# Kernel optimization log

Measured on AMD Instinct MI355X. Metric: run time of the kernel, lower is better.

## Reference

```python
import jax, jax.numpy as jnp
import numpy as np

B, S, DIM, H = 2, 2048, 2048, 16
HD = DIM // H  # head_dim = 128
EPS = 1e-6


def setup_inputs() -> dict:
    key = jax.random.key(0)
    ks = jax.random.split(key, 13)
    d = {
        'hidden_states': jax.random.normal(ks[0], (B, S, DIM), jnp.float32),
        'freqs_cos': jax.random.normal(ks[1], (1, S, 1, HD), jnp.float32),
        'freqs_sin': jax.random.normal(ks[2], (1, S, 1, HD), jnp.float32),
        'Wq': jax.random.normal(ks[3], (DIM, DIM), jnp.float32) * 0.02,
        'bq': jax.random.normal(ks[4], (DIM,), jnp.float32) * 0.02,
        'Wk': jax.random.normal(ks[5], (DIM, DIM), jnp.float32) * 0.02,
        'bk': jax.random.normal(ks[6], (DIM,), jnp.float32) * 0.02,
        'Wv': jax.random.normal(ks[7], (DIM, DIM), jnp.float32) * 0.02,
        'bv': jax.random.normal(ks[8], (DIM,), jnp.float32) * 0.02,
        'norm_q_w': jax.random.uniform(ks[9], (DIM,), jnp.float32, 0.5, 1.5),
        'norm_k_w': jax.random.uniform(ks[10], (DIM,), jnp.float32, 0.5, 1.5),
        'Wo': jax.random.normal(ks[11], (DIM, DIM), jnp.float32) * 0.02,
        'bo': jax.random.normal(ks[12], (DIM,), jnp.float32) * 0.02,
    }
    return d


def _rms_norm(x, w, eps=EPS):
    # local RMSNorm over the full inner_dim (no cross-rank reduce)
    xf = x.astype(jnp.float32)
    var = jnp.mean(xf * xf, axis=-1, keepdims=True)
    return (w * (xf * jax.lax.rsqrt(var + eps))).astype(x.dtype)


def _apply_rope(x, freqs_cos, freqs_sin):
    # x: [B,H,S,D]; freqs: [1,S,1,D] -> broadcast cos/sin at [1,1,S,D/2]
    dtype = x.dtype
    xf = x.astype(jnp.float32)
    x1 = xf[..., 0::2]
    x2 = xf[..., 1::2]
    cos = jnp.transpose(freqs_cos[..., 0::2], (0, 2, 1, 3)).astype(jnp.float32)
    sin = jnp.transpose(freqs_sin[..., 1::2], (0, 2, 1, 3)).astype(jnp.float32)
    even = x1 * cos - x2 * sin
    odd = x1 * sin + x2 * cos
    out = jnp.stack([even, odd], axis=-1).reshape(x.shape)
    return out.astype(dtype)


def reference(hidden_states, freqs_cos, freqs_sin, Wq, bq, Wk, bk, Wv, bv,
              norm_q_w, norm_k_w, Wo, bo):
    b, s, _ = hidden_states.shape
    q = hidden_states @ Wq.T + bq
    k = hidden_states @ Wk.T + bk
    v = hidden_states @ Wv.T + bv
    q = _rms_norm(q, norm_q_w)
    k = _rms_norm(k, norm_k_w)
    # [B,S,H*D] -> [B,H,S,D]
    q = q.reshape(b, s, H, HD).transpose(0, 2, 1, 3)
    k = k.reshape(b, s, H, HD).transpose(0, 2, 1, 3)
    v = v.reshape(b, s, H, HD).transpose(0, 2, 1, 3)
    q = _apply_rope(q, freqs_cos, freqs_sin)
    k = _apply_rope(k, freqs_cos, freqs_sin)
    # flash attention math (full, non-causal), scale = 1/sqrt(head_dim)
    scale = 1.0 / np.sqrt(HD).astype(np.float32)
    scores = jnp.einsum('bhqd,bhkd->bhqk', q, k) * scale
    attn = jax.nn.softmax(scores, axis=-1)
    out = jnp.einsum('bhqk,bhkd->bhqd', attn, v)
    out = out.transpose(0, 2, 1, 3).reshape(b, s, H * HD)
    return out @ Wo.T + bo
```

## Files before the change

### kernel.cpp

```cpp
#include <hip/hip_runtime.h>
#include <stdint.h>

#define DEVI __device__ __forceinline__

typedef __attribute__((ext_vector_type(8))) short bf16x8;
typedef __attribute__((ext_vector_type(4))) float f32x4;
typedef __attribute__((ext_vector_type(16))) float f32x16;
typedef __attribute__((ext_vector_type(4))) unsigned short u16x4;
typedef __attribute__((ext_vector_type(8))) unsigned short u16x8;

DEVI unsigned short f2bf(float f) {
    union { float f; unsigned u; } v; v.f = f;
    unsigned r = v.u + 0x7fffu + ((v.u >> 16) & 1u);
    return (unsigned short)(r >> 16);
}

DEVI unsigned cvtpk(float lo, float hi) {
    unsigned r;
    asm("v_cvt_pk_bf16_f32 %0, %1, %2" : "=v"(r) : "v"(lo), "v"(hi));
    return r;
}

DEVI void gload16(const void* g, void* lds) {
    __builtin_amdgcn_global_load_lds(
        (const __attribute__((address_space(1))) unsigned int*)(uintptr_t)g,
        (__attribute__((address_space(3))) unsigned int*)(unsigned int)(uintptr_t)lds,
        16, 0, 0);
}

__global__ __launch_bounds__(256) void cvt_all(
    const float* __restrict__ hs, const float* __restrict__ wq,
    const float* __restrict__ wk, const float* __restrict__ wv,
    const float* __restrict__ wo,
    unsigned short* __restrict__ o_hs, unsigned short* __restrict__ o_wq,
    unsigned short* __restrict__ o_wk, unsigned short* __restrict__ o_wv,
    unsigned short* __restrict__ o_wo) {
    const int bid = blockIdx.x;
    const float* src; unsigned short* dst; int base;
    if (bid < 2048)      { src = hs; dst = o_hs; base = bid; }
    else if (bid < 3072) { src = wq; dst = o_wq; base = bid - 2048; }
    else if (bid < 4096) { src = wk; dst = o_wk; base = bid - 3072; }
    else if (bid < 5120) { src = wv; dst = o_wv; base = bid - 4096; }
    else                 { src = wo; dst = o_wo; base = bid - 5120; }
    const int i0 = base * 1024 + threadIdx.x;
#pragma unroll
    for (int k = 0; k < 4; k++) {
        const int i = i0 + k * 256;
        float4 v = ((const float4*)src)[i];
        u16x4 pk;
        pk[0] = f2bf(v.x); pk[1] = f2bf(v.y); pk[2] = f2bf(v.z); pk[3] = f2bf(v.w);
        ((u16x4*)dst)[i] = pk;
    }
}

DEVI void gemm_pipe_core(const unsigned short* __restrict__ A,
                         const unsigned short* __restrict__ Wt,
                         int m0, int n0, char* lds,
                         f32x4 (&acc)[2][2][2][2]) {
    constexpr int K = 2048;
    const int t = threadIdx.x;
    const int w = t >> 6, l = t & 63, lr = l & 15, lk = l >> 4;
    const int wr = w >> 2, wc = w & 3;
    const int sx = lr & 7;
    const int srow = t >> 3, sseg = (t & 7) ^ (srow & 7);
    const unsigned short* aS = A + (size_t)(m0 + srow) * K + sseg * 8;
    const unsigned short* bS = Wt + (size_t)(n0 + srow) * K + sseg * 8;
    char* Bbase = lds + 32768;

#pragma unroll
    for (int qm = 0; qm < 2; qm++)
#pragma unroll
        for (int qn = 0; qn < 2; qn++)
#pragma unroll
            for (int fr = 0; fr < 2; fr++)
#pragma unroll
                for (int fc = 0; fc < 2; fc++)
                    acc[qm][qn][fr][fc] = (f32x4){0.f, 0.f, 0.f, 0.f};

    auto STAGE = [&](int tt, int u) {
        if (tt >= 32) return;
        const int k0 = tt * 64, bb = tt & 1;
        if (u < 4)
            gload16(bS + (size_t)u * 64 * K + k0, Bbase + bb * 32768 + u * 8192 + w * 1024);
        else
            gload16(aS + (size_t)(u - 4) * 64 * K + k0, lds + bb * 16384 + (u - 4) * 8192 + w * 1024);
    };

    STAGE(0, 0); STAGE(0, 1); STAGE(0, 2); STAGE(0, 3); STAGE(0, 4); STAGE(0, 5);
    STAGE(1, 0); STAGE(1, 1); STAGE(1, 2);
    asm volatile("s_waitcnt vmcnt(3)" ::: "memory");
    __builtin_amdgcn_s_barrier();

    for (int kt = 0; kt < 32; ++kt) {
        const int bb = kt & 1;
        const char* Ab = lds + bb * 16384;
        const char* Bb = Bbase + bb * 32768;
        bf16x8 a0[2][2], a1[2][2], b0[2][2], b1[2][2];
#pragma unroll
        for (int fr = 0; fr < 2; fr++)
#pragma unroll
            for (int ks = 0; ks < 2; ks++) {
                a0[fr][ks] = *(const bf16x8*)(Ab + (wr * 64 + fr * 16 + lr) * 128 +
                                              (((ks * 4 + lk) ^ sx) << 4));
                a1[fr][ks] = *(const bf16x8*)(Ab + (wr * 64 + 32 + fr * 16 + lr) * 128 +
                                              (((ks * 4 + lk) ^ sx) << 4));
            }
#pragma unroll
        for (int fc = 0; fc < 2; fc++)
#pragma unroll
            for (int ks = 0; ks < 2; ks++) {
                b0[fc][ks] = *(const bf16x8*)(Bb + (wc * 64 + fc * 16 + lr) * 128 +
                                              (((ks * 4 + lk) ^ sx) << 4));
                b1[fc][ks] = *(const bf16x8*)(Bb + (wc * 64 + 32 + fc * 16 + lr) * 128 +
                                              (((ks * 4 + lk) ^ sx) << 4));
            }
        STAGE(kt + 1, 3); STAGE(kt + 1, 4); STAGE(kt + 1, 5);
        __builtin_amdgcn_s_setprio(1);
#pragma unroll
        for (int ks = 0; ks < 2; ks++)
#pragma unroll
            for (int fr = 0; fr < 2; fr++)
#pragma unroll
                for (int fc = 0; fc < 2; fc++) {
                    acc[0][0][fr][fc] = __builtin_amdgcn_mfma_f32_16x16x32_bf16(
                        a0[fr][ks], b0[fc][ks], acc[0][0][fr][fc], 0, 0, 0);
                    acc[1][0][fr][fc] = __builtin_amdgcn_mfma_f32_16x16x32_bf16(
                        a1[fr][ks], b0[fc][ks], acc[1][0][fr][fc], 0, 0, 0);
                }
        __builtin_amdgcn_s_setprio(0);
        asm volatile("s_waitcnt lgkmcnt(0)" ::: "memory");
        __builtin_amdgcn_s_barrier();
        STAGE(kt + 2, 0); STAGE(kt + 2, 1); STAGE(kt + 2, 2);
        __builtin_amdgcn_s_setprio(1);
#pragma unroll
        for (int ks = 0; ks < 2; ks++)
#pragma unroll
            for (int fr = 0; fr < 2; fr++)
#pragma unroll
                for (int fc = 0; fc < 2; fc++) {
                    acc[0][1][fr][fc] = __builtin_amdgcn_mfma_f32_16x16x32_bf16(
                        a0[fr][ks], b1[fc][ks], acc[0][1][fr][fc], 0, 0, 0);
                    acc[1][1][fr][fc] = __builtin_amdgcn_mfma_f32_16x16x32_bf16(
                        a1[fr][ks], b1[fc][ks], acc[1][1][fr][fc], 0, 0, 0);
                }
        __builtin_amdgcn_s_setprio(0);
        if (kt < 30)       asm volatile("s_waitcnt vmcnt(3)" ::: "memory");
        else if (kt == 30) asm volatile("s_waitcnt vmcnt(0)" ::: "memory");
        __builtin_amdgcn_s_barrier();
    }
}

__global__ __launch_bounds__(512, 2) void gemm_qkv(
    const unsigned short* __restrict__ A,
    const unsigned short* __restrict__ Wq16, const unsigned short* __restrict__ Wk16,
    const unsigned short* __restrict__ Wv16,
    const float* __restrict__ bq, const float* __restrict__ bk, const float* __restrict__ bv,
    float* __restrict__ qf, float* __restrict__ kf, unsigned short* __restrict__ Vt) {
    __shared__ char Lds[98304];
    const int bid = blockIdx.x;
    const int nt = bid & 7, rem = bid >> 3;
    const int mt = rem / 3, z = rem % 3;
    const int m0 = mt * 128, n0 = nt * 256;
    const unsigned short* W = (z == 0) ? Wq16 : (z == 1) ? Wk16 : Wv16;
    const float* bias = (z == 0) ? bq : (z == 1) ? bk : bv;

    f32x4 acc[2][2][2][2];
    gemm_pipe_core(A, W, m0, n0, Lds, acc);

    const int t = threadIdx.x, w = t >> 6, l = t & 63, lr = l & 15, lk = l >> 4;
    const int wr = w >> 2, wc = w & 3;
#pragma unroll
    for (int qm = 0; qm < 2; qm++)
#pragma unroll
        for (int qn = 0; qn < 2; qn++)
#pragma unroll
            for (int fr = 0; fr < 2; fr++)
#pragma unroll
                for (int fc = 0; fc < 2; fc++) {
                    const int col = n0 + wc * 64 + qn * 32 + fc * 16 + lr;
                    const int rb = m0 + wr * 64 + qm * 32 + fr * 16 + lk * 4;
                    const float bb = bias[col];
                    if (z == 2) {
                        const int hh = col >> 7, d = col & 127;
                        const int b = rb >> 11, s = rb & 2047;
                        u16x4 pk;
#pragma unroll
                        for (int j = 0; j < 4; j++) pk[j] = f2bf(acc[qm][qn][fr][fc][j] + bb);
                        *(u16x4*)(Vt + ((size_t)((b * 16 + hh) * 128 + d)) * 2048 + s) = pk;
                    } else {
                        float* out = (z == 0) ? qf : kf;
#pragma unroll
                        for (int j = 0; j < 4; j++)
                            out[(size_t)(rb + j) * 2048 + col] = acc[qm][qn][fr][fc][j] + bb;
                    }
                }
}

__global__ __launch_bounds__(512, 2) void gemm_o(
    const unsigned short* __restrict__ A, const unsigned short* __restrict__ W16,
    const float* __restrict__ bo, float* __restrict__ out) {
    __shared__ char Lds[98304];
    const int bid = blockIdx.x;
    const int nt = bid & 7, mt = bid >> 3;
    const int m0 = mt * 128, n0 = nt * 256;

    f32x4 acc[2][2][2][2];
    gemm_pipe_core(A, W16, m0, n0, Lds, acc);

    const int t = threadIdx.x, w = t >> 6, l = t & 63, lr = l & 15, lk = l >> 4;
    const int wr = w >> 2, wc = w & 3;
#pragma unroll
    for (int qm = 0; qm < 2; qm++)
#pragma unroll
        for (int qn = 0; qn < 2; qn++)
#pragma unroll
            for (int fr = 0; fr < 2; fr++)
#pragma unroll
                for (int fc = 0; fc < 2; fc++) {
                    const int col = n0 + wc * 64 + qn * 32 + fc * 16 + lr;
                    const int rb = m0 + wr * 64 + qm * 32 + fr * 16 + lk * 4;
                    const float bb = bo[col];
#pragma unroll
                    for (int j = 0; j < 4; j++)
                        out[(size_t)(rb + j) * 2048 + col] = acc[qm][qn][fr][fc][j] + bb;
                }
}

__global__ __launch_bounds__(256) void norm_rope(
    const float* __restrict__ qf, const float* __restrict__ kf,
    const float* __restrict__ nqw, const float* __restrict__ nkw,
    const float* __restrict__ fc, const float* __restrict__ fs,
    unsigned short* __restrict__ Qr, unsigned short* __restrict__ Kr) {
    const int row = blockIdx.x;
    const int which = blockIdx.y;
    const float* in = which ? kf : qf;
    const float* wv = which ? nkw : nqw;
    unsigned short* out = which ? Kr : Qr;
    const float qs = which ? 1.0f : 0.12751744f;
    const int t = threadIdx.x;
    const float* x = in + (size_t)row * 2048 + t * 8;
    float4 v0 = ((const float4*)x)[0];
    float4 v1 = ((const float4*)x)[1];
    float xv[8] = {v0.x, v0.y, v0.z, v0.w, v1.x, v1.y, v1.z, v1.w};
    float ss = 0.f;
#pragma unroll
    for (int e = 0; e < 8; e++) ss += xv[e] * xv[e];
#pragma unroll
    for (int m = 1; m < 64; m <<= 1) ss += __shfl_xor(ss, m, 64);
    __shared__ float red[4];
    if ((t & 63) == 0) red[t >> 6] = ss;
    __syncthreads();
    const float tot = red[0] + red[1] + red[2] + red[3];
    const float r = rsqrtf(tot * (1.0f / 2048.0f) + 1e-6f);
    const int s = row & 2047, b = row >> 11;
    const int d0 = t * 8, hd0 = d0 & 127, h = d0 >> 7;
    float4 c0 = ((const float4*)(fc + s * 128 + hd0))[0];
    float4 c1 = ((const float4*)(fc + s * 128 + hd0))[1];
    float4 s0 = ((const float4*)(fs + s * 128 + hd0))[0];
    float4 s1 = ((const float4*)(fs + s * 128 + hd0))[1];
    float4 w0 = ((const float4*)(wv + d0))[0];
    float4 w1 = ((const float4*)(wv + d0))[1];
    float wn[8] = {w0.x, w0.y, w0.z, w0.w, w1.x, w1.y, w1.z, w1.w};
    float xn[8];
#pragma unroll
    for (int e = 0; e < 8; e++) xn[e] = xv[e] * wn[e] * r;
    float o[8];
    o[0] = xn[0] * c0.x - xn[1] * s0.y;  o[1] = xn[0] * s0.y + xn[1] * c0.x;
    o[2] = xn[2] * c0.z - xn[3] * s0.w;  o[3] = xn[2] * s0.w + xn[3] * c0.z;
    o[4] = xn[4] * c1.x - xn[5] * s1.y;  o[5] = xn[4] * s1.y + xn[5] * c1.x;
    o[6] = xn[6] * c1.z - xn[7] * s1.w;  o[7] = xn[6] * s1.w + xn[7] * c1.z;
    u16x8 pk;
#pragma unroll
    for (int e = 0; e < 8; e++) pk[e] = f2bf(o[e] * qs);
    *(u16x8*)(out + ((size_t)((b * 16 + h) * 2048 + s)) * 128 + hd0) = pk;
}

__global__ __launch_bounds__(256, 2) void attn(
    const unsigned short* __restrict__ Qr, const unsigned short* __restrict__ Kr,
    const unsigned short* __restrict__ Vt, unsigned short* __restrict__ Ao) {
    __shared__ unsigned short Kl[2][64 * 128];
    __shared__ unsigned short Vl[2][128 * 64];
    const int t = threadIdx.x, w = t >> 6, l = t & 63;
    const int ql = l & 31, h = l >> 5;
    const int bid = blockIdx.x;
    const int xcd = bid & 7, idx = bid >> 3;
    const int bh = xcd * 4 + (idx >> 4);
    const int q0 = (idx & 15) * 128 + w * 32;
    const int b = bh >> 4, head = bh & 15;

    const unsigned short* Qp = Qr + ((size_t)bh * 2048 + q0) * 128;
    bf16x8 qf[8];
#pragma unroll
    for (int c8 = 0; c8 < 8; c8++)
        qf[c8] = *(const bf16x8*)(Qp + ql * 128 + c8 * 16 + h * 8);

    f32x16 accO[4];
#pragma unroll
    for (int dt = 0; dt < 4; dt++)
#pragma unroll
        for (int r = 0; r < 16; r++) accO[dt][r] = 0.f;
    float mj = -1e30f, ljp = 0.f;

    const unsigned short* Kb = Kr + (size_t)bh * 2048 * 128;
    const unsigned short* Vb = Vt + (size_t)bh * 128 * 2048;
    const int krow = t >> 4, kseg = (t & 15) ^ (krow & 7);
    const int vrow = t >> 3, vseg = (t & 7) ^ (vrow & 7);

    auto STAGE = [&](int buf, int kv0) {
        char* kd = (char*)&Kl[buf][0] + w * 1024;
        char* vd = (char*)&Vl[buf][0] + w * 1024;
#pragma unroll
        for (int c = 0; c < 4; c++)
            gload16(Kb + (size_t)(kv0 + c * 16 + krow) * 128 + kseg * 8, kd + c * 4096);
#pragma unroll
        for (int c = 0; c < 4; c++)
            gload16(Vb + (size_t)(c * 32 + vrow) * 2048 + kv0 + vseg * 8, vd + c * 4096);
    };

    const int qx = ql & 7;
    STAGE(0, 0);
    __syncthreads();
    int cur = 0;
    for (int it = 0; it < 32; ++it) {
        if (it < 31) STAGE(cur ^ 1, (it + 1) * 64);
        f32x16 S0, S1;
#pragma unroll
        for (int r = 0; r < 16; r++) { S0[r] = 0.f; S1[r] = 0.f; }
        __builtin_amdgcn_s_setprio(1);
#pragma unroll
        for (int c8 = 0; c8 < 8; c8++) {
            const int sg = ((c8 * 2 + h) ^ qx) << 4;
            bf16x8 k0 = *(const bf16x8*)((const char*)&Kl[cur][0] + ql * 256 + sg);
            bf16x8 k1 = *(const bf16x8*)((const char*)&Kl[cur][0] + (32 + ql) * 256 + sg);
            S0 = __builtin_amdgcn_mfma_f32_32x32x16_bf16(k0, qf[c8], S0, 0, 0, 0);
            S1 = __builtin_amdgcn_mfma_f32_32x32x16_bf16(k1, qf[c8], S1, 0, 0, 0);
        }
        __builtin_amdgcn_s_setprio(0);
        float mloc = S0[0];
#pragma unroll
        for (int r = 1; r < 16; r++) mloc = fmaxf(mloc, S0[r]);
#pragma unroll
        for (int r = 0; r < 16; r++) mloc = fmaxf(mloc, S1[r]);
        const float mx = fmaxf(mloc, __shfl_xor(mloc, 32, 64));
        if (!__all(mx <= mj + 8.0f)) {
            const float mn = fmaxf(mj, mx);
            const float corr = exp2f(mj - mn);
            mj = mn;
            ljp *= corr;
#pragma unroll
            for (int dt = 0; dt < 4; dt++)
#pragma unroll
                for (int r = 0; r < 16; r++) accO[dt][r] *= corr;
        }
        unsigned W[16];
        float lsum = 0.f;
#pragma unroll
        for (int i = 0; i < 8; i++) {
            const float pa = exp2f(S0[2 * i] - mj);
            const float pb = exp2f(S0[2 * i + 1] - mj);
            W[i] = cvtpk(pa, pb);
            lsum += pa + pb;
        }
#pragma unroll
        for (int i = 0; i < 8; i++) {
            const float pa = exp2f(S1[2 * i] - mj);
            const float pb = exp2f(S1[2 * i + 1] - mj);
            W[8 + i] = cvtpk(pa, pb);
            lsum += pa + pb;
        }
        ljp += lsum;
#pragma unroll
        for (int c = 0; c < 2; c++) {
            unsigned X[8];
#pragma unroll
            for (int i = 0; i < 8; i++)
                X[i] = (unsigned)__shfl_xor((int)W[c * 8 + i], 32, 64);
            union U { unsigned u[4]; bf16x8 v; };
            U F, G;
            F.u[0] = h ? X[2] : W[c * 8 + 0];
            F.u[1] = h ? X[3] : W[c * 8 + 1];
            F.u[2] = h ? W[c * 8 + 2] : X[0];
            F.u[3] = h ? W[c * 8 + 3] : X[1];
            G.u[0] = h ? X[6] : W[c * 8 + 4];
            G.u[1] = h ? X[7] : W[c * 8 + 5];
            G.u[2] = h ? W[c * 8 + 6] : X[4];
            G.u[3] = h ? W[c * 8 + 7] : X[5];
            __builtin_amdgcn_s_setprio(1);
#pragma unroll
            for (int dt = 0; dt < 4; dt++) {
                const int sg = (((2 * c) * 2 + h) ^ qx) << 4;
                bf16x8 vf = *(const bf16x8*)((const char*)&Vl[cur][0] + (dt * 32 + ql) * 128 + sg);
                accO[dt] = __builtin_amdgcn_mfma_f32_32x32x16_bf16(vf, F.v, accO[dt], 0, 0, 0);
            }
#pragma unroll
            for (int dt = 0; dt < 4; dt++) {
                const int sg = (((2 * c + 1) * 2 + h) ^ qx) << 4;
                bf16x8 vf = *(const bf16x8*)((const char*)&Vl[cur][0] + (dt * 32 + ql) * 128 + sg);
                accO[dt] = __builtin_amdgcn_mfma_f32_32x32x16_bf16(vf, G.v, accO[dt], 0, 0, 0);
            }
            __builtin_amdgcn_s_setprio(0);
        }
        __syncthreads();
        cur ^= 1;
    }
    const float lj = ljp + __shfl_xor(ljp, 32, 64);
    const float inv = 1.0f / lj;
    unsigned short* ob = Ao + ((size_t)(b * 2048 + q0 + ql)) * 2048 + head * 128;
#pragma unroll
    for (int dt = 0; dt < 4; dt++)
#pragma unroll
        for (int i = 0; i < 8; i++) {
            const float a = accO[dt][2 * i] * inv;
            const float c = accO[dt][2 * i + 1] * inv;
            const int d = dt * 32 + ((2 * i) & 3) + 8 * (i >> 1) + 4 * h;
            *(unsigned*)(ob + d) = cvtpk(a, c);
        }
}

extern "C" void kernel_launch(void* const* d_in, const int* in_sizes, int n_in,
                              void* d_out, int out_size, void* d_ws, size_t ws_size,
                              hipStream_t stream) {
    const float* hs  = (const float*)d_in[0];
    const float* fc  = (const float*)d_in[1];
    const float* fs  = (const float*)d_in[2];
    const float* Wq  = (const float*)d_in[3];
    const float* bq  = (const float*)d_in[4];
    const float* Wk  = (const float*)d_in[5];
    const float* bk  = (const float*)d_in[6];
    const float* Wv  = (const float*)d_in[7];
    const float* bv  = (const float*)d_in[8];
    const float* nqw = (const float*)d_in[9];
    const float* nkw = (const float*)d_in[10];
    const float* Wo  = (const float*)d_in[11];
    const float* bo  = (const float*)d_in[12];
    float* out = (float*)d_out;

    char* p = (char*)d_ws;
    unsigned short* hs16 = (unsigned short*)p; p += (size_t)8388608 * 2;
    unsigned short* Wq16 = (unsigned short*)p; p += (size_t)4194304 * 2;
    unsigned short* Wk16 = (unsigned short*)p; p += (size_t)4194304 * 2;
    unsigned short* Wv16 = (unsigned short*)p; p += (size_t)4194304 * 2;
    unsigned short* Wo16 = (unsigned short*)p; p += (size_t)4194304 * 2;
    float* qf = (float*)p;                     p += (size_t)8388608 * 4;
    float* kf = (float*)p;                     p += (size_t)8388608 * 4;
    unsigned short* Qr = (unsigned short*)p;   p += (size_t)8388608 * 2;
    unsigned short* Kr = (unsigned short*)p;   p += (size_t)8388608 * 2;
    unsigned short* Vt = (unsigned short*)p;   p += (size_t)8388608 * 2;
    unsigned short* Ao = (unsigned short*)p;   p += (size_t)8388608 * 2;
    (void)ws_size; (void)in_sizes; (void)n_in; (void)out_size;

    cvt_all<<<6144, 256, 0, stream>>>(hs, Wq, Wk, Wv, Wo,
                                      hs16, Wq16, Wk16, Wv16, Wo16);
    gemm_qkv<<<768, 512, 0, stream>>>(hs16, Wq16, Wk16, Wv16,
                                      bq, bk, bv, qf, kf, Vt);
    norm_rope<<<dim3(4096, 2), 256, 0, stream>>>(qf, kf, nqw, nkw, fc, fs, Qr, Kr);
    attn<<<512, 256, 0, stream>>>(Qr, Kr, Vt, Ao);
    gemm_o<<<256, 512, 0, stream>>>(Ao, Wo16, bo, out);
}
```

Before: 301.0 us.

## Switch GEMM core to 32x32x16 MFMA with triple-buffered LDS pipeline

Replaces the 16x16x32 bf16 MFMA tiles in the shared QKV/O GEMM core with 32x32x16 MFMAs, which cuts the number of MFMA issues and LDS fragment loads per K-step. The LDS staging moves from double to triple buffering, prefetching two K-tiles ahead, and each 64-wide K-tile is split into two half-phases with interleaved barriers. Both GEMM epilogues are rewritten to match the 32x32 accumulator layout. The cost is more LDS per block (147 KB) and extra barriers per iteration.

Result: slower. 329.8 us (+9.6%).

```diff
diff --git a/kernel.cpp b/kernel.cpp
--- a/kernel.cpp
+++ b/kernel.cpp
@@ -56,99 +56,102 @@
 DEVI void gemm_pipe_core(const unsigned short* __restrict__ A,
                          const unsigned short* __restrict__ Wt,
                          int m0, int n0, char* lds,
-                         f32x4 (&acc)[2][2][2][2]) {
-    constexpr int K = 2048;
+                         f32x16 (&acc)[2][2]) {
+    constexpr int K = 2048, NT = 32;
     const int t = threadIdx.x;
-    const int w = t >> 6, l = t & 63, lr = l & 15, lk = l >> 4;
+    const int w = t >> 6, l = t & 63, ql = l & 31, h = l >> 5;
     const int wr = w >> 2, wc = w & 3;
-    const int sx = lr & 7;
+    const int sx = ql & 7;
     const int srow = t >> 3, sseg = (t & 7) ^ (srow & 7);
     const unsigned short* aS = A + (size_t)(m0 + srow) * K + sseg * 8;
     const unsigned short* bS = Wt + (size_t)(n0 + srow) * K + sseg * 8;
-    char* Bbase = lds + 32768;
-
-#pragma unroll
-    for (int qm = 0; qm < 2; qm++)
-#pragma unroll
-        for (int qn = 0; qn < 2; qn++)
-#pragma unroll
-            for (int fr = 0; fr < 2; fr++)
-#pragma unroll
-                for (int fc = 0; fc < 2; fc++)
-                    acc[qm][qn][fr][fc] = (f32x4){0.f, 0.f, 0.f, 0.f};
-
-    auto STAGE = [&](int tt, int u) {
-        if (tt >= 32) return;
-        const int k0 = tt * 64, bb = tt & 1;
+
+#pragma unroll
+    for (int qi = 0; qi < 2; qi++)
+#pragma unroll
+        for (int qj = 0; qj < 2; qj++)
+#pragma unroll
+            for (int r = 0; r < 16; r++) acc[qi][qj][r] = 0.f;
+
+    auto STAGE = [&](int tt, int rb, int u) {
+        if (tt >= NT) return;
+        const int k0 = tt * 64;
+        char* base = lds + rb * 49152;
         if (u < 4)
-            gload16(bS + (size_t)u * 64 * K + k0, Bbase + bb * 32768 + u * 8192 + w * 1024);
+            gload16(bS + (size_t)u * 64 * K + k0, base + 16384 + u * 8192 + w * 1024);
         else
-            gload16(aS + (size_t)(u - 4) * 64 * K + k0, lds + bb * 16384 + (u - 4) * 8192 + w * 1024);
+            gload16(aS + (size_t)(u - 4) * 64 * K + k0, base + (u - 4) * 8192 + w * 1024);
     };
 
-    STAGE(0, 0); STAGE(0, 1); STAGE(0, 2); STAGE(0, 3); STAGE(0, 4); STAGE(0, 5);
-    STAGE(1, 0); STAGE(1, 1); STAGE(1, 2);
-    asm volatile("s_waitcnt vmcnt(3)" ::: "memory");
+    for (int u = 0; u < 6; ++u) STAGE(0, 0, u);
+    for (int u = 0; u < 6; ++u) STAGE(1, 1, u);
+    asm volatile("s_waitcnt vmcnt(6)" ::: "memory");
     __builtin_amdgcn_s_barrier();
 
-    for (int kt = 0; kt < 32; ++kt) {
-        const int bb = kt & 1;
-        const char* Ab = lds + bb * 16384;
-        const char* Bb = Bbase + bb * 32768;
-        bf16x8 a0[2][2], a1[2][2], b0[2][2], b1[2][2];
-#pragma unroll
-        for (int fr = 0; fr < 2; fr++)
-#pragma unroll
-            for (int ks = 0; ks < 2; ks++) {
-                a0[fr][ks] = *(const bf16x8*)(Ab + (wr * 64 + fr * 16 + lr) * 128 +
-                                              (((ks * 4 + lk) ^ sx) << 4));
-                a1[fr][ks] = *(const bf16x8*)(Ab + (wr * 64 + 32 + fr * 16 + lr) * 128 +
-                                              (((ks * 4 + lk) ^ sx) << 4));
-            }
-#pragma unroll
-        for (int fc = 0; fc < 2; fc++)
-#pragma unroll
-            for (int ks = 0; ks < 2; ks++) {
-                b0[fc][ks] = *(const bf16x8*)(Bb + (wc * 64 + fc * 16 + lr) * 128 +
-                                              (((ks * 4 + lk) ^ sx) << 4));
-                b1[fc][ks] = *(const bf16x8*)(Bb + (wc * 64 + 32 + fc * 16 + lr) * 128 +
-                                              (((ks * 4 + lk) ^ sx) << 4));
-            }
-        STAGE(kt + 1, 3); STAGE(kt + 1, 4); STAGE(kt + 1, 5);
+    int rb = 0, rb2 = 2;
+    for (int kt = 0; kt < NT; ++kt) {
+        const char* Ab = lds + rb * 49152;
+        const char* Bb = Ab + 16384;
+        bf16x8 a[2][2], b[2][2];
+#pragma unroll
+        for (int qi = 0; qi < 2; qi++)
+#pragma unroll
+            for (int ks = 0; ks < 2; ks++)
+                a[qi][ks] = *(const bf16x8*)(Ab + (wr * 64 + qi * 32 + ql) * 128 +
+                                             (((ks * 2 + h) ^ sx) << 4));
+#pragma unroll
+        for (int qj = 0; qj < 2; qj++)
+#pragma unroll
+            for (int ks = 0; ks < 2; ks++)
+                b[qj][ks] = *(const bf16x8*)(Bb + (wc * 64 + qj * 32 + ql) * 128 +
+                                             (((ks * 2 + h) ^ sx) << 4));
+        STAGE(kt + 2, rb2, 0); STAGE(kt + 2, rb2, 1); STAGE(kt + 2, rb2, 2);
+        __builtin_amdgcn_s_barrier();
+        asm volatile("s_waitcnt lgkmcnt(0)" ::: "memory");
         __builtin_amdgcn_s_setprio(1);
 #pragma unroll
         for (int ks = 0; ks < 2; ks++)
 #pragma unroll
-            for (int fr = 0; fr < 2; fr++)
-#pragma unroll
-                for (int fc = 0; fc < 2; fc++) {
-                    acc[0][0][fr][fc] = __builtin_amdgcn_mfma_f32_16x16x32_bf16(
-                        a0[fr][ks], b0[fc][ks], acc[0][0][fr][fc], 0, 0, 0);
-                    acc[1][0][fr][fc] = __builtin_amdgcn_mfma_f32_16x16x32_bf16(
-                        a1[fr][ks], b0[fc][ks], acc[1][0][fr][fc], 0, 0, 0);
-                }
+            for (int qi = 0; qi < 2; qi++)
+#pragma unroll
+                for (int qj = 0; qj < 2; qj++)
+                    acc[qi][qj] = __builtin_amdgcn_mfma_f32_32x32x16_bf16(
+                        a[qi][ks], b[qj][ks], acc[qi][qj], 0, 0, 0);
         __builtin_amdgcn_s_setprio(0);
+        __builtin_amdgcn_s_barrier();
+#pragma unroll
+        for (int qi = 0; qi < 2; qi++)
+#pragma unroll
+            for (int ks = 0; ks < 2; ks++)
+                a[qi][ks] = *(const bf16x8*)(Ab + (wr * 64 + qi * 32 + ql) * 128 +
+                                             ((((ks + 2) * 2 + h) ^ sx) << 4));
+#pragma unroll
+        for (int qj = 0; qj < 2; qj++)
+#pragma unroll
+            for (int ks = 0; ks < 2; ks++)
+                b[qj][ks] = *(const bf16x8*)(Bb + (wc * 64 + qj * 32 + ql) * 128 +
+                                             ((((ks + 2) * 2 + h) ^ sx) << 4));
+        STAGE(kt + 2, rb2, 3); STAGE(kt + 2, rb2, 4); STAGE(kt + 2, rb2, 5);
+        __builtin_amdgcn_s_barrier();
         asm volatile("s_waitcnt lgkmcnt(0)" ::: "memory");
-        __builtin_amdgcn_s_barrier();
-        STAGE(kt + 2, 0); STAGE(kt + 2, 1); STAGE(kt + 2, 2);
         __builtin_amdgcn_s_setprio(1);
 #pragma unroll
         for (int ks = 0; ks < 2; ks++)
 #pragma unroll
-            for (int fr = 0; fr < 2; fr++)
-#pragma unroll
-                for (int fc = 0; fc < 2; fc++) {
-                    acc[0][1][fr][fc] = __builtin_amdgcn_mfma_f32_16x16x32_bf16(
-                        a0[fr][ks], b1[fc][ks], acc[0][1][fr][fc], 0, 0, 0);
-                    acc[1][1][fr][fc] = __builtin_amdgcn_mfma_f32_16x16x32_bf16(
-                        a1[fr][ks], b1[fc][ks], acc[1][1][fr][fc], 0, 0, 0);
-                }
+            for (int qi = 0; qi < 2; qi++)
+#pragma unroll
+                for (int qj = 0; qj < 2; qj++)
+                    acc[qi][qj] = __builtin_amdgcn_mfma_f32_32x32x16_bf16(
+                        a[qi][ks], b[qj][ks], acc[qi][qj], 0, 0, 0);
         __builtin_amdgcn_s_setprio(0);
-        if (kt < 30)       asm volatile("s_waitcnt vmcnt(3)" ::: "memory");
+        if (kt < 30)       asm volatile("s_waitcnt vmcnt(6)" ::: "memory");
         else if (kt == 30) asm volatile("s_waitcnt vmcnt(0)" ::: "memory");
         __builtin_amdgcn_s_barrier();
+        rb  = (rb  + 1 == 3) ? 0 : rb  + 1;
+        rb2 = (rb2 + 1 == 3) ? 0 : rb2 + 1;
     }
 }
+
 
 __global__ __launch_bounds__(512, 2) void gemm_qkv(
     const unsigned short* __restrict__ A,
@@ -156,7 +159,7 @@
     const unsigned short* __restrict__ Wv16,
     const float* __restrict__ bq, const float* __restrict__ bk, const float* __restrict__ bv,
     float* __restrict__ qf, float* __restrict__ kf, unsigned short* __restrict__ Vt) {
-    __shared__ char Lds[98304];
+    __shared__ char Lds[147456];
     const int bid = blockIdx.x;
     const int nt = bid & 7, rem = bid >> 3;
     const int mt = rem / 3, z = rem % 3;
@@ -164,66 +167,68 @@
     const unsigned short* W = (z == 0) ? Wq16 : (z == 1) ? Wk16 : Wv16;
     const float* bias = (z == 0) ? bq : (z == 1) ? bk : bv;
 
-    f32x4 acc[2][2][2][2];
+    f32x16 acc[2][2];
     gemm_pipe_core(A, W, m0, n0, Lds, acc);
 
-    const int t = threadIdx.x, w = t >> 6, l = t & 63, lr = l & 15, lk = l >> 4;
+    const int t = threadIdx.x, w = t >> 6, l = t & 63, ql = l & 31, h = l >> 5;
     const int wr = w >> 2, wc = w & 3;
 #pragma unroll
-    for (int qm = 0; qm < 2; qm++)
-#pragma unroll
-        for (int qn = 0; qn < 2; qn++)
-#pragma unroll
-            for (int fr = 0; fr < 2; fr++)
-#pragma unroll
-                for (int fc = 0; fc < 2; fc++) {
-                    const int col = n0 + wc * 64 + qn * 32 + fc * 16 + lr;
-                    const int rb = m0 + wr * 64 + qm * 32 + fr * 16 + lk * 4;
-                    const float bb = bias[col];
-                    if (z == 2) {
-                        const int hh = col >> 7, d = col & 127;
-                        const int b = rb >> 11, s = rb & 2047;
-                        u16x4 pk;
-#pragma unroll
-                        for (int j = 0; j < 4; j++) pk[j] = f2bf(acc[qm][qn][fr][fc][j] + bb);
-                        *(u16x4*)(Vt + ((size_t)((b * 16 + hh) * 128 + d)) * 2048 + s) = pk;
-                    } else {
-                        float* out = (z == 0) ? qf : kf;
-#pragma unroll
-                        for (int j = 0; j < 4; j++)
-                            out[(size_t)(rb + j) * 2048 + col] = acc[qm][qn][fr][fc][j] + bb;
-                    }
+    for (int qi = 0; qi < 2; qi++)
+#pragma unroll
+        for (int qj = 0; qj < 2; qj++) {
+            const int col = n0 + wc * 64 + qj * 32 + ql;
+            const float bb = bias[col];
+            if (z == 2) {
+                const int hh = col >> 7, d = col & 127;
+#pragma unroll
+                for (int rq = 0; rq < 4; rq++) {
+                    const int row = m0 + wr * 64 + qi * 32 + 8 * rq + 4 * h;
+                    const int b = row >> 11, s = row & 2047;
+                    u16x4 pk;
+#pragma unroll
+                    for (int j = 0; j < 4; j++) pk[j] = f2bf(acc[qi][qj][rq * 4 + j] + bb);
+                    *(u16x4*)(Vt + ((size_t)((b * 16 + hh) * 128 + d)) * 2048 + s) = pk;
                 }
+            } else {
+                float* out = (z == 0) ? qf : kf;
+#pragma unroll
+                for (int rq = 0; rq < 4; rq++) {
+                    const int row = m0 + wr * 64 + qi * 32 + 8 * rq + 4 * h;
+#pragma unroll
+                    for (int j = 0; j < 4; j++)
+                        out[(size_t)(row + j) * 2048 + col] = acc[qi][qj][rq * 4 + j] + bb;
+                }
+            }
+        }
 }
 
 __global__ __launch_bounds__(512, 2) void gemm_o(
     const unsigned short* __restrict__ A, const unsigned short* __restrict__ W16,
     const float* __restrict__ bo, float* __restrict__ out) {
-    __shared__ char Lds[98304];
+    __shared__ char Lds[147456];
     const int bid = blockIdx.x;
     const int nt = bid & 7, mt = bid >> 3;
     const int m0 = mt * 128, n0 = nt * 256;
 
-    f32x4 acc[2][2][2][2];
+    f32x16 acc[2][2];
     gemm_pipe_core(A, W16, m0, n0, Lds, acc);
 
-    const int t = threadIdx.x, w = t >> 6, l = t & 63, lr = l & 15, lk = l >> 4;
+    const int t = threadIdx.x, w = t >> 6, l = t & 63, ql = l & 31, h = l >> 5;
     const int wr = w >> 2, wc = w & 3;
 #pragma unroll
-    for (int qm = 0; qm < 2; qm++)
-#pragma unroll
-        for (int qn = 0; qn < 2; qn++)
-#pragma unroll
-            for (int fr = 0; fr < 2; fr++)
-#pragma unroll
-                for (int fc = 0; fc < 2; fc++) {
-                    const int col = n0 + wc * 64 + qn * 32 + fc * 16 + lr;
-                    const int rb = m0 + wr * 64 + qm * 32 + fr * 16 + lk * 4;
-                    const float bb = bo[col];
-#pragma unroll
-                    for (int j = 0; j < 4; j++)
-                        out[(size_t)(rb + j) * 2048 + col] = acc[qm][qn][fr][fc][j] + bb;
-                }
+    for (int qi = 0; qi < 2; qi++)
+#pragma unroll
+        for (int qj = 0; qj < 2; qj++) {
+            const int col = n0 + wc * 64 + qj * 32 + ql;
+            const float bb = bo[col];
+#pragma unroll
+            for (int rq = 0; rq < 4; rq++) {
+                const int row = m0 + wr * 64 + qi * 32 + 8 * rq + 4 * h;
+#pragma unroll
+                for (int j = 0; j < 4; j++)
+                    out[(size_t)(row + j) * 2048 + col] = acc[qi][qj][rq * 4 + j] + bb;
+            }
+        }
 }
 
 __global__ __launch_bounds__(256) void norm_rope(
```

## Single-buffer V and stagger K/V prefetch to fit three blocks per CU

Applied to the files above, without the earlier changes.

The attention kernel drops the V double buffer, cutting LDS from 64 KB to 48 KB, and raises the launch-bounds occupancy hint from 2 to 3 blocks per CU. K is now prefetched two tiles ahead while V is loaded one tile ahead, after the PV MMAs finish. Explicit vmcnt waits and barriers order the loads and compute. The aim is more resident waves to hide latency, at the cost of a tighter register budget (possible spills) and extra barriers per iteration, with V load latency exposed behind only the QK and softmax phase.

New measurement: 324.3 us. 1.08x slower.

```diff
diff --git a/kernel.cpp b/kernel.cpp
--- a/kernel.cpp
+++ b/kernel.cpp
@@ -275,11 +275,11 @@
     *(u16x8*)(out + ((size_t)((b * 16 + h) * 2048 + s)) * 128 + hd0) = pk;
 }
 
-__global__ __launch_bounds__(256, 2) void attn(
+__global__ __launch_bounds__(256, 3) void attn(
     const unsigned short* __restrict__ Qr, const unsigned short* __restrict__ Kr,
     const unsigned short* __restrict__ Vt, unsigned short* __restrict__ Ao) {
     __shared__ unsigned short Kl[2][64 * 128];
-    __shared__ unsigned short Vl[2][128 * 64];
+    __shared__ unsigned short Vl[128 * 64];
     const int t = threadIdx.x, w = t >> 6, l = t & 63;
     const int ql = l & 31, h = l >> 5;
     const int bid = blockIdx.x;
@@ -306,23 +306,29 @@
     const int krow = t >> 4, kseg = (t & 15) ^ (krow & 7);
     const int vrow = t >> 3, vseg = (t & 7) ^ (vrow & 7);
 
-    auto STAGE = [&](int buf, int kv0) {
-        char* kd = (char*)&Kl[buf][0] + w * 1024;
-        char* vd = (char*)&Vl[buf][0] + w * 1024;
+    auto STAGE_K = [&](int it) {
+        if (it >= 32) return;
+        char* kd = (char*)&Kl[it & 1][0] + w * 1024;
 #pragma unroll
         for (int c = 0; c < 4; c++)
-            gload16(Kb + (size_t)(kv0 + c * 16 + krow) * 128 + kseg * 8, kd + c * 4096);
+            gload16(Kb + (size_t)(it * 64 + c * 16 + krow) * 128 + kseg * 8, kd + c * 4096);
+    };
+    auto STAGE_V = [&](int it) {
+        if (it >= 32) return;
+        char* vd = (char*)&Vl[0] + w * 1024;
 #pragma unroll
         for (int c = 0; c < 4; c++)
-            gload16(Vb + (size_t)(c * 32 + vrow) * 2048 + kv0 + vseg * 8, vd + c * 4096);
+            gload16(Vb + (size_t)(c * 32 + vrow) * 2048 + it * 64 + vseg * 8, vd + c * 4096);
     };
 
+    STAGE_K(0); STAGE_V(0); STAGE_K(1);
+
     const int qx = ql & 7;
-    STAGE(0, 0);
-    __syncthreads();
-    int cur = 0;
     for (int it = 0; it < 32; ++it) {
-        if (it < 31) STAGE(cur ^ 1, (it + 1) * 64);
+        if (it < 31) asm volatile("s_waitcnt vmcnt(8)" ::: "memory");
+        else         asm volatile("s_waitcnt vmcnt(4)" ::: "memory");
+        __builtin_amdgcn_s_barrier();
+        const char* Kc = (const char*)&Kl[it & 1][0];
         f32x16 S0, S1;
 #pragma unroll
         for (int r = 0; r < 16; r++) { S0[r] = 0.f; S1[r] = 0.f; }
@@ -330,8 +336,8 @@
 #pragma unroll
         for (int c8 = 0; c8 < 8; c8++) {
             const int sg = ((c8 * 2 + h) ^ qx) << 4;
-            bf16x8 k0 = *(const bf16x8*)((const char*)&Kl[cur][0] + ql * 256 + sg);
-            bf16x8 k1 = *(const bf16x8*)((const char*)&Kl[cur][0] + (32 + ql) * 256 + sg);
+            bf16x8 k0 = *(const bf16x8*)(Kc + ql * 256 + sg);
+            bf16x8 k1 = *(const bf16x8*)(Kc + (32 + ql) * 256 + sg);
             S0 = __builtin_amdgcn_mfma_f32_32x32x16_bf16(k0, qf[c8], S0, 0, 0, 0);
             S1 = __builtin_amdgcn_mfma_f32_32x32x16_bf16(k1, qf[c8], S1, 0, 0, 0);
         }
@@ -369,6 +375,9 @@
             lsum += pa + pb;
         }
         ljp += lsum;
+        if (it < 31) asm volatile("s_waitcnt vmcnt(4)" ::: "memory");
+        else         asm volatile("s_waitcnt vmcnt(0)" ::: "memory");
+        __builtin_amdgcn_s_barrier();
 #pragma unroll
         for (int c = 0; c < 2; c++) {
             unsigned X[8];
@@ -389,19 +398,21 @@
 #pragma unroll
             for (int dt = 0; dt < 4; dt++) {
                 const int sg = (((2 * c) * 2 + h) ^ qx) << 4;
-                bf16x8 vf = *(const bf16x8*)((const char*)&Vl[cur][0] + (dt * 32 + ql) * 128 + sg);
+                bf16x8 vf = *(const bf16x8*)((const char*)&Vl[0] + (dt * 32 + ql) * 128 + sg);
                 accO[dt] = __builtin_amdgcn_mfma_f32_32x32x16_bf16(vf, F.v, accO[dt], 0, 0, 0);
             }
 #pragma unroll
             for (int dt = 0; dt < 4; dt++) {
                 const int sg = (((2 * c + 1) * 2 + h) ^ qx) << 4;
-                bf16x8 vf = *(const bf16x8*)((const char*)&Vl[cur][0] + (dt * 32 + ql) * 128 + sg);
+                bf16x8 vf = *(const bf16x8*)((const char*)&Vl[0] + (dt * 32 + ql) * 128 + sg);
                 accO[dt] = __builtin_amdgcn_mfma_f32_32x32x16_bf16(vf, G.v, accO[dt], 0, 0, 0);
             }
             __builtin_amdgcn_s_setprio(0);
         }
-        __syncthreads();
-        cur ^= 1;
+        asm volatile("s_waitcnt lgkmcnt(0)" ::: "memory");
+        __builtin_amdgcn_s_barrier();
+        STAGE_V(it + 1);
+        STAGE_K(it + 2);
     }
     const float lj = ljp + __shfl_xor(ljp, 32, 64);
     const float inv = 1.0f / lj;
```
